# Kernel optimization log

Hardware: AMD Instinct MI355X
Metric: run time of the kernel (lower is better)

Reference implementation:

```python
import jax, jax.numpy as jnp
import numpy as np

D_MODEL = 512
N_HEADS = 8
D_HEAD = D_MODEL // N_HEADS
MAX_LEN = 5000


def _make_pe():
    # sinusoidal table for relative positions -MAX_LEN..+MAX_LEN
    pos = np.arange(-MAX_LEN, MAX_LEN + 1, dtype=np.float32)[:, None]
    div = np.exp(np.arange(0, D_MODEL, 2, dtype=np.float32) * (-np.log(10000.0) / D_MODEL))
    pe = np.zeros((2 * MAX_LEN + 1, D_MODEL), dtype=np.float32)
    pe[:, 0::2] = np.sin(pos * div)
    pe[:, 1::2] = np.cos(pos * div)
    return jnp.asarray(pe)


def setup_inputs() -> dict:
    key = jax.random.key(0)
    ks = jax.random.split(key, 10)
    B, S = 8, 512
    xavier = lambda k: jax.random.uniform(k, (D_MODEL, D_MODEL), jnp.float32,
                                          -np.sqrt(6.0 / (2 * D_MODEL)), np.sqrt(6.0 / (2 * D_MODEL)))
    return {
        "x": jax.random.normal(ks[0], (B, S, D_MODEL), jnp.float32),
        "wq": xavier(ks[1]), "bq": jnp.zeros((D_MODEL,), jnp.float32),
        "wk": xavier(ks[2]), "bk": jnp.zeros((D_MODEL,), jnp.float32),
        "wv": xavier(ks[3]), "bv": jnp.zeros((D_MODEL,), jnp.float32),
        "wo": xavier(ks[4]), "bo": jnp.zeros((D_MODEL,), jnp.float32),
        "wr": xavier(ks[5]),
        "u": jnp.zeros((N_HEADS, D_HEAD), jnp.float32),
        "v_bias": jnp.zeros((N_HEADS, D_HEAD), jnp.float32),
        "pe": _make_pe(),
    }


def reference(x, wq, bq, wk, bk, wv, bv, wo, bo, wr, u, v_bias, pe):
    B, S, D = x.shape
    H, dh = N_HEADS, D_HEAD
    scale = dh ** -0.5

    # projections (torch Linear: x @ W.T + b) -> [B, H, S, dh]
    def proj(w, b):
        return (x @ w.T + b).reshape(B, S, H, dh).transpose(0, 2, 1, 3)
    q = proj(wq, bq)
    k = proj(wk, bk)
    v = proj(wv, bv)

    # relative position encodings: rel[i,j] = pe[clip(j-i) + MAX_LEN]
    pos = jnp.arange(S)
    rel_idx = jnp.clip(pos[None, :] - pos[:, None], -MAX_LEN, MAX_LEN) + MAX_LEN
    rel_pos = pe[rel_idx]                              # [S, S, D]
    rel_proj = (rel_pos @ wr.T).reshape(S, S, H, dh)   # [S, S, H, dh]
    rel_proj = rel_proj.transpose(2, 0, 1, 3)          # [H, S, S, dh]

    content = jnp.einsum('bhid,bhjd->bhij', q + u[None, :, None, :], k)
    position = jnp.einsum('bhid,hijd->bhij', q + v_bias[None, :, None, :], rel_proj)
    attn = jax.nn.softmax((content + position) * scale, axis=-1)

    out = jnp.einsum('bhij,bhjd->bhid', attn, v)       # [B, H, S, dh]
    out = out.transpose(0, 2, 1, 3).reshape(B, S, D)
    return out @ wo.T + bo
```

## Files before the change

### kernel.cpp

```cpp
#include <hip/hip_runtime.h>
#include <math.h>

#define DM 512
#define NH 8
#define DH 64
#define SEQ 512
#define BATCH 8
#define MR 1023
#define PE_OFF 4489

typedef float4 f4;
typedef __attribute__((ext_vector_type(8))) short bf16x8;
typedef __attribute__((ext_vector_type(4))) float f32x4;
typedef __attribute__((ext_vector_type(8))) unsigned short u16x8;
typedef __attribute__((ext_vector_type(4))) unsigned short u16x4;

__device__ __forceinline__ unsigned short f2bf(float f) {
    unsigned x = __float_as_uint(f);
    unsigned r = x + 0x7fffu + ((x >> 16) & 1u);
    return (unsigned short)(r >> 16);
}
__device__ __forceinline__ float bf2f(unsigned short h) {
    return __uint_as_float(((unsigned)h) << 16);
}
__device__ __forceinline__ f32x4 mfma16(bf16x8 a, bf16x8 b, f32x4 c) {
    return __builtin_amdgcn_mfma_f32_16x16x32_bf16(a, b, c, 0, 0, 0);
}

__device__ __forceinline__ void cvt8(const float* __restrict__ src,
                                     unsigned short* __restrict__ hi,
                                     unsigned short* __restrict__ lo, int i) {
    f4 a = *(const f4*)&src[i];
    f4 b = *(const f4*)&src[i + 4];
    float v[8] = {a.x, a.y, a.z, a.w, b.x, b.y, b.z, b.w};
    u16x8 h, l;
#pragma unroll
    for (int j = 0; j < 8; ++j) {
        unsigned short hb = f2bf(v[j]);
        h[j] = hb;
        l[j] = f2bf(v[j] - bf2f(hb));
    }
    *(u16x8*)&hi[i] = h;
    *(u16x8*)&lo[i] = l;
}

__global__ __launch_bounds__(256) void cvt_all_kernel(
    const float* __restrict__ x,
    const float* __restrict__ w0, const float* __restrict__ w1,
    const float* __restrict__ w2, const float* __restrict__ w3,
    const float* __restrict__ w4, const float* __restrict__ pe,
    unsigned short* __restrict__ xh, unsigned short* __restrict__ xl,
    unsigned short* __restrict__ wb,
    unsigned short* __restrict__ peh, unsigned short* __restrict__ pel)
{
    const int bid = blockIdx.x, tid = threadIdx.x;
    if (bid < 1024) {
        cvt8(x, xh, xl, (bid * 256 + tid) * 8);
    } else if (bid < 1664) {
        const int wsel = (bid - 1024) >> 7;
        const float* src = (wsel == 0) ? w0 : (wsel == 1) ? w1 :
                           (wsel == 2) ? w2 : (wsel == 3) ? w3 : w4;
        unsigned short* hi = wb + (size_t)wsel * 524288;
        cvt8(src, hi, hi + 262144, (((bid - 1024) & 127) * 256 + tid) * 8);
    } else {
        const int i = ((bid - 1664) * 256 + tid) * 8;
        if (i < 523776) cvt8(pe, peh, pel, i);
    }
}

__device__ __forceinline__ void gemm_core128(
    const unsigned short* __restrict__ Ah, const unsigned short* __restrict__ Al,
    const unsigned short* __restrict__ Wh, const unsigned short* __restrict__ Wl,
    int m0, int n0, f32x4 acc[4][2],
    unsigned short* LAh, unsigned short* LAl,
    unsigned short* LBh, unsigned short* LBl)
{
    const int tid = threadIdx.x;
    const int lane = tid & 63, wid = tid >> 6;
    const int wm = (wid >> 1) << 6, wn = (wid & 1) << 5;
    const int ar = tid >> 1, ac = (tid & 1) << 4;
    const int br = tid >> 2, bc = (tid & 3) << 3;
    const int fr = lane & 15, g = lane >> 4;

#pragma unroll
    for (int i = 0; i < 4; ++i)
#pragma unroll
        for (int j = 0; j < 2; ++j)
            acc[i][j] = (f32x4){0.f, 0.f, 0.f, 0.f};

    const size_t arow = (size_t)(m0 + ar) * DM + ac;
    const size_t wrow = (size_t)(n0 + br) * DM + bc;

    for (int k0 = 0; k0 < DM; k0 += 32) {
        u16x8 a0 = *(const u16x8*)&Ah[arow + k0];
        u16x8 a1 = *(const u16x8*)&Ah[arow + k0 + 8];
        u16x8 a2 = *(const u16x8*)&Al[arow + k0];
        u16x8 a3 = *(const u16x8*)&Al[arow + k0 + 8];
        u16x8 b0 = *(const u16x8*)&Wh[wrow + k0];
        u16x8 b1 = *(const u16x8*)&Wl[wrow + k0];
        if (k0) __syncthreads();
        *(u16x8*)&LAh[ar * 40 + ac] = a0;
        *(u16x8*)&LAh[ar * 40 + ac + 8] = a1;
        *(u16x8*)&LAl[ar * 40 + ac] = a2;
        *(u16x8*)&LAl[ar * 40 + ac + 8] = a3;
        *(u16x8*)&LBh[br * 40 + bc] = b0;
        *(u16x8*)&LBl[br * 40 + bc] = b1;
        __syncthreads();

        bf16x8 a_h[4], a_l[4], b_h[2], b_l[2];
#pragma unroll
        for (int mi = 0; mi < 4; ++mi) {
            a_h[mi] = *(const bf16x8*)&LAh[(wm + (mi << 4) + fr) * 40 + (g << 3)];
            a_l[mi] = *(const bf16x8*)&LAl[(wm + (mi << 4) + fr) * 40 + (g << 3)];
        }
#pragma unroll
        for (int ni = 0; ni < 2; ++ni) {
            b_h[ni] = *(const bf16x8*)&LBh[(wn + (ni << 4) + fr) * 40 + (g << 3)];
            b_l[ni] = *(const bf16x8*)&LBl[(wn + (ni << 4) + fr) * 40 + (g << 3)];
        }
#pragma unroll
        for (int mi = 0; mi < 4; ++mi)
#pragma unroll
            for (int ni = 0; ni < 2; ++ni) {
                acc[mi][ni] = mfma16(a_h[mi], b_h[ni], acc[mi][ni]);
                acc[mi][ni] = mfma16(a_h[mi], b_l[ni], acc[mi][ni]);
                acc[mi][ni] = mfma16(a_l[mi], b_h[ni], acc[mi][ni]);
            }
    }
}

#define GEMM_LDS \
    __shared__ unsigned short LAh[128 * 40], LAl[128 * 40]; \
    __shared__ unsigned short LBh[64 * 40], LBl[64 * 40];

__global__ __launch_bounds__(256) void qkv_rm_kernel(
    const unsigned short* __restrict__ xh, const unsigned short* __restrict__ xl,
    const unsigned short* __restrict__ wb,
    const unsigned short* __restrict__ peh, const unsigned short* __restrict__ pel,
    const float* __restrict__ bq, const float* __restrict__ bk,
    const float* __restrict__ bv, const float* __restrict__ u,
    const float* __restrict__ vb,
    unsigned short* __restrict__ qh, unsigned short* __restrict__ ql,
    unsigned short* __restrict__ kh, unsigned short* __restrict__ kl,
    unsigned short* __restrict__ vth, unsigned short* __restrict__ vtl,
    unsigned short* __restrict__ rmh, unsigned short* __restrict__ rml,
    float* __restrict__ rc)
{
    GEMM_LDS
    const int bid = blockIdx.x;
    const int tid = threadIdx.x, lane = tid & 63, wid = tid >> 6;
    const int wm = (wid >> 1) << 6, wn = (wid & 1) << 5;
    const int fr = lane & 15, g = lane >> 4;

    if (bid < 64) {
        const int n0 = (bid & 7) << 6, m0 = (bid >> 3) << 7;
        const unsigned short* wrh = wb + 4 * 524288;
        const unsigned short* wrl = wrh + 262144;
        f32x4 acc[4][2];
        gemm_core128(peh, pel, wrh, wrl, m0, n0, acc, LAh, LAl, LBh, LBl);

        const int h = n0 >> 6;
        float part[4][4];
        float wgt[2];
#pragma unroll
        for (int ni = 0; ni < 2; ++ni) {
            const int d = wn + (ni << 4) + fr;
            wgt[ni] = vb[(h << 6) + d] - u[(h << 6) + d];
        }
#pragma unroll
        for (int mi = 0; mi < 4; ++mi)
#pragma unroll
            for (int r = 0; r < 4; ++r) part[mi][r] = 0.f;

#pragma unroll
        for (int ni = 0; ni < 2; ++ni) {
            const int n_g = n0 + wn + (ni << 4) + fr;
            const int d = n_g & 63;
#pragma unroll
            for (int mi = 0; mi < 4; ++mi)
#pragma unroll
                for (int r = 0; r < 4; ++r) {
                    const int dd = m0 + wm + (mi << 4) + (g << 2) + r;
                    const float val = acc[mi][ni][r];
                    const size_t o = (((size_t)h << 10) + dd) * DH + d;
                    const unsigned short hb = f2bf(val);
                    rmh[o] = hb;
                    rml[o] = f2bf(val - bf2f(hb));
                    part[mi][r] = fmaf(wgt[ni], val, part[mi][r]);
                }
        }

        __syncthreads();
        float* cbuf = (float*)LAh;
#pragma unroll
        for (int mi = 0; mi < 4; ++mi)
#pragma unroll
            for (int r = 0; r < 4; ++r) {
                float v = part[mi][r];
#pragma unroll
                for (int off = 8; off; off >>= 1) v += __shfl_xor(v, off, 16);
                if (fr == 0)
                    cbuf[((wid & 1) << 7) + wm + (mi << 4) + (g << 2) + r] = v;
            }
        __syncthreads();
        if (tid < 128)
            rc[((size_t)h << 10) + m0 + tid] = cbuf[tid] + cbuf[128 + tid];
        return;
    }

    const int t = bid - 64;
    const int wsel = t >> 8;
    const int rest = t & 255;
    const int n0 = (rest & 7) << 6, m0 = (rest >> 3) << 7;
    const unsigned short* Wh = wb + (size_t)wsel * 524288;
    const unsigned short* Wl = Wh + 262144;
    f32x4 acc[4][2];
    gemm_core128(xh, xl, Wh, Wl, m0, n0, acc, LAh, LAl, LBh, LBl);

    const float* bias = (wsel == 0) ? bq : (wsel == 1) ? bk : bv;

    if (wsel < 2) {
        unsigned short* oh = (wsel == 0) ? qh : kh;
        unsigned short* ol = (wsel == 0) ? ql : kl;
#pragma unroll
        for (int ni = 0; ni < 2; ++ni) {
            const int n_g = n0 + wn + (ni << 4) + fr;
            float bvv = bias[n_g] + ((wsel == 0) ? u[n_g] : 0.f);
            const int h = n_g >> 6, d = n_g & 63;
#pragma unroll
            for (int mi = 0; mi < 4; ++mi)
#pragma unroll
                for (int r = 0; r < 4; ++r) {
                    const int m_g = m0 + wm + (mi << 4) + (g << 2) + r;
                    const int b = m_g >> 9, s = m_g & 511;
                    const float val = acc[mi][ni][r] + bvv;
                    const size_t o = ((size_t)(b * NH + h) * SEQ + s) * DH + d;
                    const unsigned short hb = f2bf(val);
                    oh[o] = hb;
                    ol[o] = f2bf(val - bf2f(hb));
                }
        }
    } else {
#pragma unroll
        for (int ni = 0; ni < 2; ++ni) {
            const int n_g = n0 + wn + (ni << 4) + fr;
            const float bvv = bias[n_g];
            const int h = n_g >> 6, d = n_g & 63;
#pragma unroll
            for (int mi = 0; mi < 4; ++mi) {
                const int m_b = m0 + wm + (mi << 4) + (g << 2);
                const int b = m_b >> 9, s = m_b & 511;
                u16x4 hv, lv;
#pragma unroll
                for (int r = 0; r < 4; ++r) {
                    const float val = acc[mi][ni][r] + bvv;
                    hv[r] = f2bf(val);
                    lv[r] = f2bf(val - bf2f(hv[r]));
                }
                const size_t o = ((size_t)(b * NH + h) * DH + d) * SEQ + s;
                *(u16x4*)&vth[o] = hv;
                *(u16x4*)&vtl[o] = lv;
            }
        }
    }
}

__global__ __launch_bounds__(256) void out_kernel(
    const unsigned short* __restrict__ cth, const unsigned short* __restrict__ ctl,
    const unsigned short* __restrict__ woh, const unsigned short* __restrict__ wol,
    const float* __restrict__ bo, float* __restrict__ out)
{
    GEMM_LDS
    const int n0 = blockIdx.x << 6, m0 = blockIdx.y << 7;
    f32x4 acc[4][2];
    gemm_core128(cth, ctl, woh, wol, m0, n0, acc, LAh, LAl, LBh, LBl);

    const int tid = threadIdx.x, lane = tid & 63, wid = tid >> 6;
    const int wm = (wid >> 1) << 6, wn = (wid & 1) << 5;
    const int fr = lane & 15, g = lane >> 4;
#pragma unroll
    for (int ni = 0; ni < 2; ++ni) {
        const int n_g = n0 + wn + (ni << 4) + fr;
        const float bvv = bo[n_g];
#pragma unroll
        for (int mi = 0; mi < 4; ++mi)
#pragma unroll
            for (int r = 0; r < 4; ++r) {
                const int m_g = m0 + wm + (mi << 4) + (g << 2) + r;
                out[(size_t)m_g * DM + n_g] = acc[mi][ni][r] + bvv;
            }
    }
}

__global__ __launch_bounds__(256) void attn_kernel(
    const unsigned short* __restrict__ qh_g, const unsigned short* __restrict__ ql_g,
    const unsigned short* __restrict__ kh_g, const unsigned short* __restrict__ kl_g,
    const unsigned short* __restrict__ vh_g, const unsigned short* __restrict__ vl_g,
    const unsigned short* __restrict__ rmh, const unsigned short* __restrict__ rml,
    const float* __restrict__ rc,
    unsigned short* __restrict__ cth, unsigned short* __restrict__ ctl)
{
    __shared__ unsigned short Kh[64][72], Kl[64][72], Vh[64][72], Vl[64][72];
    __shared__ unsigned short Pdd[4][16][84];
    __shared__ float Pt[4][16][68];

    const int tid = threadIdx.x;
    const int lane = tid & 63, wid = tid >> 6;
    const int g = lane >> 4, c = lane & 15;
    const int i0 = blockIdx.x << 6;
    const int h = blockIdx.y, b = blockIdx.z;
    const int R0 = i0 + (wid << 4);
    const size_t bh = (size_t)(b * NH + h) * (SEQ * DH);

    const int srow = tid >> 3;
    const int sch = (tid & 7) << 3;

    bf16x8 qhf[2], qlf[2];
#pragma unroll
    for (int ks = 0; ks < 2; ++ks) {
        const size_t qo = bh + (size_t)(R0 + c) * DH + (ks << 5) + (g << 3);
        qhf[ks] = *(const bf16x8*)&qh_g[qo];
        qlf[ks] = *(const bf16x8*)&ql_g[qo];
    }

    f32x4 Oacc[4];
#pragma unroll
    for (int nf = 0; nf < 4; ++nf) Oacc[nf] = (f32x4){0.f, 0.f, 0.f, 0.f};
    float m_r[4] = {-3e38f, -3e38f, -3e38f, -3e38f};
    float l_r[4] = {0.f, 0.f, 0.f, 0.f};

    const float* rch = rc + (h << 10);
    const unsigned short* rmhh = rmh + ((size_t)h << 16);
    const unsigned short* rmlh = rml + ((size_t)h << 16);

    u16x8 p0, p1, p2, p3, p4, p5, p6, p7;
    {
        const size_t kb = bh + (size_t)srow * DH + sch;
        p0 = *(const u16x8*)&kh_g[kb];
        p1 = *(const u16x8*)&kh_g[kb + 32 * DH];
        p2 = *(const u16x8*)&kl_g[kb];
        p3 = *(const u16x8*)&kl_g[kb + 32 * DH];
        const size_t vb_ = bh + (size_t)srow * SEQ + sch;
        p4 = *(const u16x8*)&vh_g[vb_];
        p5 = *(const u16x8*)&vh_g[vb_ + 32 * SEQ];
        p6 = *(const u16x8*)&vl_g[vb_];
        p7 = *(const u16x8*)&vl_g[vb_ + 32 * SEQ];
    }

    for (int jt = 0; jt < 8; ++jt) {
        const int j0 = jt << 6;
        __syncthreads();
        *(u16x8*)&Kh[srow][sch] = p0;
        *(u16x8*)&Kh[srow + 32][sch] = p1;
        *(u16x8*)&Kl[srow][sch] = p2;
        *(u16x8*)&Kl[srow + 32][sch] = p3;
        *(u16x8*)&Vh[srow][sch] = p4;
        *(u16x8*)&Vh[srow + 32][sch] = p5;
        *(u16x8*)&Vl[srow][sch] = p6;
        *(u16x8*)&Vl[srow + 32][sch] = p7;
        __syncthreads();
        if (jt < 7) {
            const int jn = j0 + 64;
            const size_t kb = bh + (size_t)(jn + srow) * DH + sch;
            p0 = *(const u16x8*)&kh_g[kb];
            p1 = *(const u16x8*)&kh_g[kb + 32 * DH];
            p2 = *(const u16x8*)&kl_g[kb];
            p3 = *(const u16x8*)&kl_g[kb + 32 * DH];
            const size_t vb_ = bh + (size_t)srow * SEQ + jn + sch;
            p4 = *(const u16x8*)&vh_g[vb_];
            p5 = *(const u16x8*)&vh_g[vb_ + 32 * SEQ];
            p6 = *(const u16x8*)&vl_g[vb_];
            p7 = *(const u16x8*)&vl_g[vb_ + 32 * SEQ];
        }

        __builtin_amdgcn_s_setprio(1);
        f32x4 accs[4];
#pragma unroll
        for (int nf = 0; nf < 4; ++nf) accs[nf] = (f32x4){0.f, 0.f, 0.f, 0.f};
#pragma unroll
        for (int ks = 0; ks < 2; ++ks)
#pragma unroll
            for (int nf = 0; nf < 4; ++nf) {
                bf16x8 b_h = *(const bf16x8*)&Kh[(nf << 4) + c][(ks << 5) + (g << 3)];
                bf16x8 b_l = *(const bf16x8*)&Kl[(nf << 4) + c][(ks << 5) + (g << 3)];
                accs[nf] = mfma16(qhf[ks], b_h, accs[nf]);
                accs[nf] = mfma16(qhf[ks], b_l, accs[nf]);
                accs[nf] = mfma16(qlf[ks], b_h, accs[nf]);
            }

        const int base_g = j0 - R0 + 496;
#pragma unroll
        for (int f = 0; f < 5; ++f) {
            f32x4 ap = (f32x4){0.f, 0.f, 0.f, 0.f};
#pragma unroll
            for (int ks = 0; ks < 2; ++ks) {
                const size_t ro = (size_t)(base_g + (f << 4) + c) * DH
                                + (ks << 5) + (g << 3);
                bf16x8 b_h = *(const bf16x8*)&rmhh[ro];
                bf16x8 b_l = *(const bf16x8*)&rmlh[ro];
                ap = mfma16(qhf[ks], b_h, ap);
                ap = mfma16(qhf[ks], b_l, ap);
                ap = mfma16(qlf[ks], b_h, ap);
            }
            const float rcv = rch[base_g + (f << 4) + c];
#pragma unroll
            for (int r = 0; r < 4; ++r)
                Pdd[wid][(g << 2) + r][(f << 4) + c] = f2bf(ap[r] + rcv);
        }
        __builtin_amdgcn_s_setprio(0);

#pragma unroll
        for (int r = 0; r < 4; ++r) {
            const int irow = (g << 2) + r;
            float sc[4];
#pragma unroll
            for (int nf = 0; nf < 4; ++nf) {
                const int ddl = (nf << 4) + c - irow + 15;
                sc[nf] = (accs[nf][r] + bf2f(Pdd[wid][irow][ddl])) * 0.125f;
            }
            float mt = fmaxf(fmaxf(sc[0], sc[1]), fmaxf(sc[2], sc[3]));
#pragma unroll
            for (int off = 8; off; off >>= 1) mt = fmaxf(mt, __shfl_xor(mt, off, 16));
            const float mn = fmaxf(m_r[r], mt);
            const float alpha = __expf(m_r[r] - mn);
            m_r[r] = mn;
            float rs = 0.f;
#pragma unroll
            for (int nf = 0; nf < 4; ++nf) {
                const float p = __expf(sc[nf] - mn);
                Pt[wid][irow][(nf << 4) + c] = p;
                rs += p;
            }
#pragma unroll
            for (int off = 8; off; off >>= 1) rs += __shfl_xor(rs, off, 16);
            l_r[r] = l_r[r] * alpha + rs;
#pragma unroll
            for (int nf = 0; nf < 4; ++nf) Oacc[nf][r] *= alpha;
        }

        __builtin_amdgcn_s_setprio(1);
#pragma unroll
        for (int ks = 0; ks < 2; ++ks) {
            f4 pv0 = *(const f4*)&Pt[wid][c][(ks << 5) + (g << 3)];
            f4 pv1 = *(const f4*)&Pt[wid][c][(ks << 5) + (g << 3) + 4];
            float pv[8] = {pv0.x, pv0.y, pv0.z, pv0.w, pv1.x, pv1.y, pv1.z, pv1.w};
            bf16x8 ph, pl;
#pragma unroll
            for (int e = 0; e < 8; ++e) {
                const unsigned short hb = f2bf(pv[e]);
                ph[e] = (short)hb;
                pl[e] = (short)f2bf(pv[e] - bf2f(hb));
            }
#pragma unroll
            for (int nf = 0; nf < 4; ++nf) {
                bf16x8 v_h = *(const bf16x8*)&Vh[(nf << 4) + c][(ks << 5) + (g << 3)];
                bf16x8 v_l = *(const bf16x8*)&Vl[(nf << 4) + c][(ks << 5) + (g << 3)];
                Oacc[nf] = mfma16(ph, v_h, Oacc[nf]);
                Oacc[nf] = mfma16(ph, v_l, Oacc[nf]);
                Oacc[nf] = mfma16(pl, v_h, Oacc[nf]);
            }
        }
        __builtin_amdgcn_s_setprio(0);
    }

    float inv[4];
#pragma unroll
    for (int r = 0; r < 4; ++r) inv[r] = 1.f / l_r[r];
#pragma unroll
    for (int nf = 0; nf < 4; ++nf)
#pragma unroll
        for (int r = 0; r < 4; ++r) {
            const float val = Oacc[nf][r] * inv[r];
            const int s = R0 + (g << 2) + r;
            const int d = (h << 6) + (nf << 4) + c;
            const size_t o = ((size_t)(b * SEQ) + s) * DM + d;
            const unsigned short hb = f2bf(val);
            cth[o] = hb;
            ctl[o] = f2bf(val - bf2f(hb));
        }
}

extern "C" void kernel_launch(void* const* d_in, const int* in_sizes, int n_in,
                              void* d_out, int out_size, void* d_ws, size_t ws_size,
                              hipStream_t stream)
{
    const float* x  = (const float*)d_in[0];
    const float* wq = (const float*)d_in[1];
    const float* bq = (const float*)d_in[2];
    const float* wk = (const float*)d_in[3];
    const float* bk = (const float*)d_in[4];
    const float* wv = (const float*)d_in[5];
    const float* bv = (const float*)d_in[6];
    const float* wo = (const float*)d_in[7];
    const float* bo = (const float*)d_in[8];
    const float* wr = (const float*)d_in[9];
    const float* u  = (const float*)d_in[10];
    const float* vb = (const float*)d_in[11];
    const float* pe = (const float*)d_in[12];
    float* out = (float*)d_out;
    unsigned short* us = (unsigned short*)d_ws;

    unsigned short* xh  = us;
    unsigned short* xl  = us + 2097152;
    unsigned short* wb  = us + 4194304;
    unsigned short* peh = us + 6815744;
    unsigned short* pel = us + 7340032;
    unsigned short* qh  = us + 7864320;
    unsigned short* ql  = us + 9961472;
    unsigned short* kh  = us + 12058624;
    unsigned short* kl  = us + 14155776;
    unsigned short* vth = us + 16252928;
    unsigned short* vtl = us + 18350080;
    unsigned short* rmh = us + 20447232;
    unsigned short* rml = us + 20971520;
    unsigned short* cth = us + 21495808;
    unsigned short* ctl = us + 23592960;
    float* rc = (float*)(us + 25690112);

    unsigned short* woh = wb + 3 * 524288;
    unsigned short* wol = woh + 262144;

    dim3 blk(256);
    cvt_all_kernel<<<1920, blk, 0, stream>>>(x, wq, wk, wv, wo, wr,
                                             pe + (size_t)PE_OFF * DM,
                                             xh, xl, wb, peh, pel);
    qkv_rm_kernel<<<832, blk, 0, stream>>>(xh, xl, wb, peh, pel,
                                           bq, bk, bv, u, vb,
                                           qh, ql, kh, kl, vth, vtl,
                                           rmh, rml, rc);
    attn_kernel<<<dim3(8, 8, 8), blk, 0, stream>>>(qh, ql, kh, kl, vth, vtl,
                                                   rmh, rml, rc, cth, ctl);
    out_kernel<<<dim3(8, 32), blk, 0, stream>>>(cth, ctl, woh, wol, bo, out);
}
```

Baseline: 125.0 us.

## Load GEMM tiles with global_load_lds and pre-swizzled global layout

The shared GEMM core now moves A/B tiles straight from global memory into LDS with the global_load_lds builtin, instead of going through registers. LDS tiles drop the padded stride of 40 for a dense stride of 32. To avoid LDS bank conflicts without padding, the producers (the conversion kernel and the attention context writer) store bf16 data with an XOR swizzle on 8-element column groups, and the readers apply the matching swizzle. This removes register staging and VGPR pressure, but it couples the data layout across kernels, so every consumer of the swizzled buffers must agree on it.

```diff
diff --git a/kernel.cpp b/kernel.cpp
--- a/kernel.cpp
+++ b/kernel.cpp
@@ -26,22 +26,29 @@
 __device__ __forceinline__ f32x4 mfma16(bf16x8 a, bf16x8 b, f32x4 c) {
     return __builtin_amdgcn_mfma_f32_16x16x32_bf16(a, b, c, 0, 0, 0);
 }
-
-__device__ __forceinline__ void cvt8(const float* __restrict__ src,
-                                     unsigned short* __restrict__ hi,
-                                     unsigned short* __restrict__ lo, int i) {
+__device__ __forceinline__ void gll16(const unsigned short* g, unsigned short* l) {
+    __builtin_amdgcn_global_load_lds(
+        (const __attribute__((address_space(1))) unsigned int*)g,
+        (__attribute__((address_space(3))) unsigned int*)l, 16, 0, 0);
+}
+
+__device__ __forceinline__ void cvt8s(const float* __restrict__ src,
+                                      unsigned short* __restrict__ hi,
+                                      unsigned short* __restrict__ lo, int i) {
+    const int row = i >> 9, col = i & 511;
+    const int j = (i & ~511) | (col ^ (((row >> 1) & 3) << 3));
     f4 a = *(const f4*)&src[i];
     f4 b = *(const f4*)&src[i + 4];
     float v[8] = {a.x, a.y, a.z, a.w, b.x, b.y, b.z, b.w};
     u16x8 h, l;
 #pragma unroll
-    for (int j = 0; j < 8; ++j) {
-        unsigned short hb = f2bf(v[j]);
-        h[j] = hb;
-        l[j] = f2bf(v[j] - bf2f(hb));
-    }
-    *(u16x8*)&hi[i] = h;
-    *(u16x8*)&lo[i] = l;
+    for (int e = 0; e < 8; ++e) {
+        unsigned short hb = f2bf(v[e]);
+        h[e] = hb;
+        l[e] = f2bf(v[e] - bf2f(hb));
+    }
+    *(u16x8*)&hi[j] = h;
+    *(u16x8*)&lo[j] = l;
 }
 
 __global__ __launch_bounds__(256) void cvt_all_kernel(
@@ -55,16 +62,16 @@
 {
     const int bid = blockIdx.x, tid = threadIdx.x;
     if (bid < 1024) {
-        cvt8(x, xh, xl, (bid * 256 + tid) * 8);
+        cvt8s(x, xh, xl, (bid * 256 + tid) * 8);
     } else if (bid < 1664) {
         const int wsel = (bid - 1024) >> 7;
         const float* src = (wsel == 0) ? w0 : (wsel == 1) ? w1 :
                            (wsel == 2) ? w2 : (wsel == 3) ? w3 : w4;
         unsigned short* hi = wb + (size_t)wsel * 524288;
-        cvt8(src, hi, hi + 262144, (((bid - 1024) & 127) * 256 + tid) * 8);
+        cvt8s(src, hi, hi + 262144, (((bid - 1024) & 127) * 256 + tid) * 8);
     } else {
         const int i = ((bid - 1664) * 256 + tid) * 8;
-        if (i < 523776) cvt8(pe, peh, pel, i);
+        if (i < 523776) cvt8s(pe, peh, pel, i);
     }
 }
 
@@ -78,9 +85,9 @@
     const int tid = threadIdx.x;
     const int lane = tid & 63, wid = tid >> 6;
     const int wm = (wid >> 1) << 6, wn = (wid & 1) << 5;
-    const int ar = tid >> 1, ac = (tid & 1) << 4;
-    const int br = tid >> 2, bc = (tid & 3) << 3;
     const int fr = lane & 15, g = lane >> 4;
+    const int crow = lane >> 2;
+    const int ccol = (lane & 3) << 3;
 
 #pragma unroll
     for (int i = 0; i < 4; ++i)
@@ -88,35 +95,34 @@
         for (int j = 0; j < 2; ++j)
             acc[i][j] = (f32x4){0.f, 0.f, 0.f, 0.f};
 
-    const size_t arow = (size_t)(m0 + ar) * DM + ac;
-    const size_t wrow = (size_t)(n0 + br) * DM + bc;
+    const size_t ga1 = (size_t)(m0 + (wid << 4) + crow) * DM + ccol;
+    const size_t ga2 = ga1 + (size_t)64 * DM;
+    const size_t gb  = (size_t)(n0 + (wid << 4) + crow) * DM + ccol;
+    const int lbase = wid << 9;
+    const int cswz = (g ^ ((fr >> 1) & 3)) << 3;
 
     for (int k0 = 0; k0 < DM; k0 += 32) {
-        u16x8 a0 = *(const u16x8*)&Ah[arow + k0];
-        u16x8 a1 = *(const u16x8*)&Ah[arow + k0 + 8];
-        u16x8 a2 = *(const u16x8*)&Al[arow + k0];
-        u16x8 a3 = *(const u16x8*)&Al[arow + k0 + 8];
-        u16x8 b0 = *(const u16x8*)&Wh[wrow + k0];
-        u16x8 b1 = *(const u16x8*)&Wl[wrow + k0];
         if (k0) __syncthreads();
-        *(u16x8*)&LAh[ar * 40 + ac] = a0;
-        *(u16x8*)&LAh[ar * 40 + ac + 8] = a1;
-        *(u16x8*)&LAl[ar * 40 + ac] = a2;
-        *(u16x8*)&LAl[ar * 40 + ac + 8] = a3;
-        *(u16x8*)&LBh[br * 40 + bc] = b0;
-        *(u16x8*)&LBl[br * 40 + bc] = b1;
+        gll16(Ah + ga1 + k0, LAh + lbase);
+        gll16(Ah + ga2 + k0, LAh + lbase + 2048);
+        gll16(Al + ga1 + k0, LAl + lbase);
+        gll16(Al + ga2 + k0, LAl + lbase + 2048);
+        gll16(Wh + gb + k0, LBh + lbase);
+        gll16(Wl + gb + k0, LBl + lbase);
         __syncthreads();
 
         bf16x8 a_h[4], a_l[4], b_h[2], b_l[2];
 #pragma unroll
         for (int mi = 0; mi < 4; ++mi) {
-            a_h[mi] = *(const bf16x8*)&LAh[(wm + (mi << 4) + fr) * 40 + (g << 3)];
-            a_l[mi] = *(const bf16x8*)&LAl[(wm + (mi << 4) + fr) * 40 + (g << 3)];
+            const int ro = (wm + (mi << 4) + fr) << 5;
+            a_h[mi] = *(const bf16x8*)&LAh[ro + cswz];
+            a_l[mi] = *(const bf16x8*)&LAl[ro + cswz];
         }
 #pragma unroll
         for (int ni = 0; ni < 2; ++ni) {
-            b_h[ni] = *(const bf16x8*)&LBh[(wn + (ni << 4) + fr) * 40 + (g << 3)];
-            b_l[ni] = *(const bf16x8*)&LBl[(wn + (ni << 4) + fr) * 40 + (g << 3)];
+            const int ro = (wn + (ni << 4) + fr) << 5;
+            b_h[ni] = *(const bf16x8*)&LBh[ro + cswz];
+            b_l[ni] = *(const bf16x8*)&LBl[ro + cswz];
         }
 #pragma unroll
         for (int mi = 0; mi < 4; ++mi)
@@ -130,8 +136,8 @@
 }
 
 #define GEMM_LDS \
-    __shared__ unsigned short LAh[128 * 40], LAl[128 * 40]; \
-    __shared__ unsigned short LBh[64 * 40], LBl[64 * 40];
+    __shared__ unsigned short LAh[128 * 32], LAl[128 * 32]; \
+    __shared__ unsigned short LBh[64 * 32], LBl[64 * 32];
 
 __global__ __launch_bounds__(256) void qkv_rm_kernel(
     const unsigned short* __restrict__ xh, const unsigned short* __restrict__ xl,
@@ -471,9 +477,11 @@
 #pragma unroll
         for (int r = 0; r < 4; ++r) {
             const float val = Oacc[nf][r] * inv[r];
-            const int s = R0 + (g << 2) + r;
+            const int sr_ = (g << 2) + r;
+            const int s = R0 + sr_;
             const int d = (h << 6) + (nf << 4) + c;
-            const size_t o = ((size_t)(b * SEQ) + s) * DM + d;
+            const int dsw = d ^ (((sr_ >> 1) & 3) << 3);
+            const size_t o = ((size_t)(b * SEQ) + s) * DM + dsw;
             const unsigned short hb = f2bf(val);
             cth[o] = hb;
             ctl[o] = f2bf(val - bf2f(hb));
```

Result: faster. 120.2 us (-3.8%).
